# Kernel tuning notes

Measured on AMD Instinct MI355X. Metric: run time of the kernel, lower is better.

The kernel has to match this reference:

```python
import jax, jax.numpy as jnp
import numpy as np

D_MODEL = 512
N_HEADS = 8
BLOCK = 512
D_HEAD = D_MODEL // N_HEADS
SCALE = D_HEAD ** -0.5


def _linear_params(key, d_in, d_out):
    kw, kb = jax.random.split(key)
    bound = 1.0 / np.sqrt(d_in)
    w = jax.random.uniform(kw, (d_in, d_out), jnp.float32, -bound, bound)
    b = jax.random.uniform(kb, (d_out,), jnp.float32, -bound, bound)
    return w, b


def setup_inputs() -> dict:
    key = jax.random.key(0)
    keys = jax.random.split(key, 10)
    x = jax.random.normal(keys[0], (4, 8192, D_MODEL), jnp.float32)
    names = ["lq", "lk", "lv", "lo", "gq", "gk", "gv", "go"]
    inp = {"x": x}
    for i, n in enumerate(names):
        w, b = _linear_params(keys[1 + i], D_MODEL, D_MODEL)
        inp[n + "_w"] = w
        inp[n + "_b"] = b
    gw, gb = _linear_params(keys[9], 2 * D_MODEL, D_MODEL)
    inp["gate_w"] = gw
    inp["gate_b"] = gb
    return inp


def _attend(q, k, v):
    # q,k,v: (..., L, H, Dh) -> (..., L, H, Dh)
    scores = jnp.einsum("...qhd,...khd->...hqk", q, k) * SCALE
    probs = jax.nn.softmax(scores, axis=-1)
    return jnp.einsum("...hqk,...khd->...qhd", probs, v)


def reference(x, lq_w, lq_b, lk_w, lk_b, lv_w, lv_b, lo_w, lo_b,
              gq_w, gq_b, gk_w, gk_b, gv_w, gv_b, go_w, go_b,
              gate_w, gate_b):
    B, S, D = x.shape
    nb = S // BLOCK
    xb = x.reshape(B, nb, BLOCK, D)

    def heads(t, L_axes):
        return t.reshape(t.shape[:-1] + (N_HEADS, D_HEAD))

    # block-local attention (all blocks batched)
    Q = heads(xb @ lq_w + lq_b, None)  # (B, nb, bs, H, Dh)
    K = heads(xb @ lk_w + lk_b, None)
    V = heads(xb @ lv_w + lv_b, None)
    loc = _attend(Q, K, V).reshape(B, nb, BLOCK, D)
    local_out = (loc @ lo_w + lo_b).reshape(B, S, D)

    # pooled block summaries: AdaptiveAvgPool1d(1) == mean over block length
    pooled = xb.mean(axis=2)  # (B, nb, D)
    Qg = heads(pooled @ gq_w + gq_b, None)  # (B, nb, H, Dh)
    Kg = heads(pooled @ gk_w + gk_b, None)
    Vg = heads(pooled @ gv_w + gv_b, None)
    glob = _attend(Qg, Kg, Vg).reshape(B, nb, D)
    glob = glob @ go_w + go_b  # (B, nb, D)

    # broadcast each block summary to its tokens
    global_out = jnp.repeat(glob, BLOCK, axis=1)  # (B, S, D)

    gate_in = jnp.concatenate([local_out, global_out], axis=-1)
    gate = jax.nn.sigmoid(gate_in @ gate_w + gate_b)
    return gate * local_out + (1.0 - gate) * global_out
```

## Files before the change

kernel.cpp:

```cpp
#include <hip/hip_runtime.h>
#include <math.h>

typedef unsigned short u16;
typedef short s16;
typedef u16 u16x8 __attribute__((ext_vector_type(8)));
typedef u16 u16x4 __attribute__((ext_vector_type(4)));
typedef s16 s16x8 __attribute__((ext_vector_type(8)));
typedef float f32x4 __attribute__((ext_vector_type(4)));
typedef unsigned u32x4 __attribute__((ext_vector_type(4)));

__device__ __forceinline__ float b2f(u16 u) { return __uint_as_float(((unsigned)u) << 16); }
__device__ __forceinline__ u16 f2b(float f) {
  unsigned x = __float_as_uint(f);
  unsigned r = x + 0x7fffu + ((x >> 16) & 1u);
  return (u16)(r >> 16);
}
__device__ __forceinline__ unsigned cvtpk(float a, float b) {
  unsigned r;
  asm("v_cvt_pk_bf16_f32 %0, %1, %2" : "=v"(r) : "v"(a), "v"(b));
  return r;
}
union PkH { u32x4 w; s16x8 h; };
union Pk2 { unsigned w[2]; u16x4 h; };

#define SCALE 0.125f
#define SCLG2E 0.1803368801111137f
#define DM 512
#define NTOK 32768

typedef __attribute__((address_space(1))) unsigned int as1_u32;
typedef __attribute__((address_space(3))) unsigned int as3_u32;
__device__ __forceinline__ void gl2lds16(const u16* g, u16* s) {
  __builtin_amdgcn_global_load_lds((as1_u32*)g, (as3_u32*)s, 16, 0, 0);
}

__global__ __launch_bounds__(256)
void conv_psum(const float* __restrict__ X, u16* __restrict__ Xb,
               float* __restrict__ Psum)
{
  __shared__ float ps[4][512];
  const int tid = threadIdx.x;
  const int c8 = (tid & 63) * 8;
  const int rg = tid >> 6;
  const size_t tok0 = (size_t)blockIdx.x * 64;
  f32x4 s0 = {0.f, 0.f, 0.f, 0.f}, s1 = {0.f, 0.f, 0.f, 0.f};
  for (int it = 0; it < 16; ++it) {
    const size_t tok = tok0 + it * 4 + rg;
    const float* xp = X + tok * DM + c8;
    f32x4 a = *(const f32x4*)xp;
    f32x4 b = *(const f32x4*)(xp + 4);
    Pk2 p0, p1;
    p0.w[0] = cvtpk(a[0], a[1]); p0.w[1] = cvtpk(a[2], a[3]);
    p1.w[0] = cvtpk(b[0], b[1]); p1.w[1] = cvtpk(b[2], b[3]);
    *(u16x4*)(Xb + tok * DM + c8)     = p0.h;
    *(u16x4*)(Xb + tok * DM + c8 + 4) = p1.h;
    s0 += a; s1 += b;
  }
  *(f32x4*)&ps[rg][c8]     = s0;
  *(f32x4*)&ps[rg][c8 + 4] = s1;
  __syncthreads();
#pragma unroll
  for (int i = 0; i < 2; ++i) {
    const int col = tid + i * 256;
    Psum[(size_t)blockIdx.x * DM + col] =
        ps[0][col] + ps[1][col] + ps[2][col] + ps[3][col];
  }
}

__global__ __launch_bounds__(256)
void pool_prep(const float* __restrict__ Psum, u16* __restrict__ PB)
{
  const int g = blockIdx.x, tid = threadIdx.x;
#pragma unroll
  for (int i = 0; i < 2; ++i) {
    const int col = tid + i * 256;
    float v = 0.f;
#pragma unroll
    for (int s = 0; s < 8; ++s) v += Psum[(size_t)(g * 8 + s) * DM + col];
    PB[(size_t)g * DM + col] = f2b(v * (1.f / 512.f));
  }
}

__global__ __launch_bounds__(256)
void trans_w(const float* w0, const float* w1, const float* w2, const float* w3,
             const float* w4, const float* w5, const float* w6, const float* w7,
             const float* w8, const float* w9, u16* __restrict__ WT)
{
  __shared__ float t[32][33];
  const int z = blockIdx.z;
  const float* W = (z == 0) ? w0 : (z == 1) ? w1 : (z == 2) ? w2 : (z == 3) ? w3 :
                   (z == 4) ? w4 : (z == 5) ? w5 : (z == 6) ? w6 : (z == 7) ? w7 :
                   (z == 8) ? w8 : w9;
  u16* D = WT + (size_t)z * DM * DM;
  const int tx = threadIdx.x & 31, ty = threadIdx.x >> 5;
  const int n0 = blockIdx.x * 32, k0 = blockIdx.y * 32;
#pragma unroll
  for (int j = 0; j < 4; ++j)
    t[ty + j * 8][tx] = W[(size_t)(k0 + ty + j * 8) * DM + n0 + tx];
  __syncthreads();
#pragma unroll
  for (int j = 0; j < 4; ++j)
    D[(size_t)(n0 + ty + j * 8) * DM + k0 + tx] = f2b(t[tx][ty + j * 8]);
}

__global__ __launch_bounds__(256)
void conv_w(const float* __restrict__ W, u16* __restrict__ D)
{
  const size_t i = ((size_t)blockIdx.x * 256 + threadIdx.x) * 8;
  f32x4 a = *(const f32x4*)(W + i);
  f32x4 b = *(const f32x4*)(W + i + 4);
  Pk2 p0, p1;
  p0.w[0] = cvtpk(a[0], a[1]); p0.w[1] = cvtpk(a[2], a[3]);
  p1.w[0] = cvtpk(b[0], b[1]); p1.w[1] = cvtpk(b[2], b[3]);
  *(u16x4*)(D + i)     = p0.h;
  *(u16x4*)(D + i + 4) = p1.h;
}

__global__ __launch_bounds__(256)
void bc_kernel(const float* __restrict__ go_b, const float* __restrict__ gate_w,
               const float* __restrict__ gate_b, float* __restrict__ bc)
{
  __shared__ float red[8][32];
  const int tid = threadIdx.x;
  const int jj = tid & 31, part = tid >> 5;
  const int j = blockIdx.x * 32 + jj;
  float p = 0.f;
#pragma unroll
  for (int i = 0; i < 64; ++i) {
    const int k = part * 64 + i;
    p = fmaf(go_b[k], gate_w[(size_t)(512 + k) * DM + j], p);
  }
  red[part][jj] = p;
  __syncthreads();
  if (tid < 32) {
    float v = gate_b[blockIdx.x * 32 + tid];
#pragma unroll
    for (int s = 0; s < 8; ++s) v += red[s][tid];
    bc[blockIdx.x * 32 + tid] = v;
  }
}

__global__ __launch_bounds__(256)
void gemm_qkv(const u16* __restrict__ A,
              const u16* __restrict__ WTq, const u16* __restrict__ WTk,
              const u16* __restrict__ WTv,
              const float* __restrict__ bq, const float* __restrict__ bk,
              const float* __restrict__ bv,
              u16* __restrict__ Qb, u16* __restrict__ Kb, u16* __restrict__ VT)
{
  __shared__ u16 As[2][128 * 64];
  __shared__ u16 Bs[2][128 * 64];
  const int tid = threadIdx.x;
  const int w = tid >> 6, l = tid & 63;
  const int l15 = l & 15, gl = l >> 4;
  const int wm = w >> 1, wn = w & 1;

  const int H = blockIdx.y * 12 + blockIdx.x;
  const int xcd = H & 7, i = H >> 3;
  const int mt = xcd * 32 + i / 12;
  const int nt = i % 12;
  const int sel = nt >> 2;
  const int m0 = mt * 128;
  const int n0 = (nt & 3) * 128;

  const u16* Wt = (sel == 0) ? WTq : (sel == 1) ? WTk : WTv;
  const float* bias = (sel == 0) ? bq : (sel == 1) ? bk : bv;

  const int srow = l >> 3;
  const int scol = ((l & 7) ^ (srow & 7)) * 8;
  const u16* Ag = A  + (size_t)(m0 + w * 32 + srow) * DM + scol;
  const u16* Bg = Wt + (size_t)(n0 + w * 32 + srow) * DM + scol;

  auto stage = [&](int t, int b) {
    const int k0 = t * 64;
#pragma unroll
    for (int c = 0; c < 4; ++c) {
      gl2lds16(Ag + (size_t)(c * 8) * DM + k0, &As[b][(w * 32 + c * 8) * 64]);
      gl2lds16(Bg + (size_t)(c * 8) * DM + k0, &Bs[b][(w * 32 + c * 8) * 64]);
    }
  };

  f32x4 acc[4][4];
#pragma unroll
  for (int ii = 0; ii < 4; ++ii)
#pragma unroll
    for (int j = 0; j < 4; ++j) acc[ii][j] = {0.f, 0.f, 0.f, 0.f};

  const int xorv = l15 & 7;
  stage(0, 0);
#pragma unroll
  for (int t = 0; t < 8; ++t) {
    if (t < 7) {
      stage(t + 1, (t + 1) & 1);
      asm volatile("s_waitcnt vmcnt(8)" ::: "memory");
    } else {
      asm volatile("s_waitcnt vmcnt(0)" ::: "memory");
    }
    __builtin_amdgcn_s_barrier();
    __builtin_amdgcn_sched_barrier(0);
    const int b = t & 1;
#pragma unroll
    for (int kd = 0; kd < 2; ++kd) {
      const int go = ((gl + 4 * kd) ^ xorv) * 8;
      s16x8 af[4], bfr[4];
#pragma unroll
      for (int f = 0; f < 4; ++f) {
        af[f]  = *(const s16x8*)&As[b][(wm * 64 + f * 16 + l15) * 64 + go];
        bfr[f] = *(const s16x8*)&Bs[b][(wn * 64 + f * 16 + l15) * 64 + go];
      }
      if (sel == 2) {
#pragma unroll
        for (int fm = 0; fm < 4; ++fm)
#pragma unroll
          for (int fn = 0; fn < 4; ++fn)
            acc[fm][fn] = __builtin_amdgcn_mfma_f32_16x16x32_bf16(
                af[fm], bfr[fn], acc[fm][fn], 0, 0, 0);
      } else {
#pragma unroll
        for (int fm = 0; fm < 4; ++fm)
#pragma unroll
          for (int fn = 0; fn < 4; ++fn)
            acc[fm][fn] = __builtin_amdgcn_mfma_f32_16x16x32_bf16(
                bfr[fn], af[fm], acc[fm][fn], 0, 0, 0);
      }
    }
    __builtin_amdgcn_s_barrier();
  }

  if (sel == 2) {
#pragma unroll
    for (int fn = 0; fn < 4; ++fn) {
      const int n = n0 + wn * 64 + fn * 16 + l15;
      const float bn = bias[n];
      const int d = n & 63, ghn = n >> 6;
#pragma unroll
      for (int fm = 0; fm < 4; ++fm) {
        const int m = m0 + wm * 64 + fm * 16 + gl * 4;
        const int f = (m & 63) >> 4;
        const int pos = ((f >> 1) << 5) | (gl << 3) | ((f & 1) << 2);
        Pk2 p;
        p.w[0] = cvtpk(acc[fm][fn][0] + bn, acc[fm][fn][1] + bn);
        p.w[1] = cvtpk(acc[fm][fn][2] + bn, acc[fm][fn][3] + bn);
        *(u16x4*)(VT + ((size_t)(((m >> 9) * 8 + ghn) * 64 + d)) * 512
                     + ((m & 511) >> 6) * 64 + pos) = p.h;
      }
    }
  } else {
    u16* Cb = (sel == 0) ? Qb : Kb;
    const float sc = (sel == 0) ? SCLG2E : 1.0f;
#pragma unroll
    for (int fm = 0; fm < 4; ++fm) {
      const int m = m0 + wm * 64 + fm * 16 + l15;
#pragma unroll
      for (int fn = 0; fn < 4; ++fn) {
        const int nb = n0 + wn * 64 + fn * 16 + gl * 4;
        f32x4 b4 = *(const f32x4*)&bias[nb];
        f32x4 v = (acc[fm][fn] + b4) * sc;
        Pk2 p;
        p.w[0] = cvtpk(v[0], v[1]);
        p.w[1] = cvtpk(v[2], v[3]);
        *(u16x4*)(Cb + (size_t)m * DM + nb) = p.h;
      }
    }
  }
}

template<int EPI>
__global__ __launch_bounds__(256)
void gemm_mfma(const u16* __restrict__ A, const u16* __restrict__ Wt,
               const float* __restrict__ bias, u16* __restrict__ Cb,
               float* __restrict__ Cf, float outscale,
               const float* __restrict__ GG)
{
  __shared__ u16 As[2][128 * 64];
  __shared__ u16 Bs[2][128 * 64];
  const int tid = threadIdx.x;
  const int w = tid >> 6, l = tid & 63;
  const int l15 = l & 15, gl = l >> 4;
  const int wm = w >> 1, wn = w & 1;

  int mt, nt;
  if (gridDim.y == 256) {
    const int H = blockIdx.y * 4 + blockIdx.x;
    const int xcd = H & 7, i = H >> 3;
    mt = xcd * 32 + (i >> 2);
    nt = i & 3;
  } else {
    mt = blockIdx.y; nt = blockIdx.x;
  }
  const int m0 = mt * 128, n0 = nt * 128;

  const int srow = l >> 3;
  const int scol = ((l & 7) ^ (srow & 7)) * 8;
  const u16* Ag = A  + (size_t)(m0 + w * 32 + srow) * DM + scol;
  const u16* Bg = Wt + (size_t)(n0 + w * 32 + srow) * DM + scol;

  auto stage = [&](int t, int b) {
    const int k0 = t * 64;
#pragma unroll
    for (int c = 0; c < 4; ++c) {
      gl2lds16(Ag + (size_t)(c * 8) * DM + k0, &As[b][(w * 32 + c * 8) * 64]);
      gl2lds16(Bg + (size_t)(c * 8) * DM + k0, &Bs[b][(w * 32 + c * 8) * 64]);
    }
  };

  f32x4 acc[4][4];
#pragma unroll
  for (int i = 0; i < 4; ++i)
#pragma unroll
    for (int j = 0; j < 4; ++j) acc[i][j] = {0.f, 0.f, 0.f, 0.f};

  const int xorv = l15 & 7;
  stage(0, 0);
#pragma unroll
  for (int t = 0; t < 8; ++t) {
    if (t < 7) {
      stage(t + 1, (t + 1) & 1);
      asm volatile("s_waitcnt vmcnt(8)" ::: "memory");
    } else {
      asm volatile("s_waitcnt vmcnt(0)" ::: "memory");
    }
    __builtin_amdgcn_s_barrier();
    __builtin_amdgcn_sched_barrier(0);
    const int b = t & 1;
#pragma unroll
    for (int kd = 0; kd < 2; ++kd) {
      const int go = ((gl + 4 * kd) ^ xorv) * 8;
      s16x8 af[4], bfr[4];
#pragma unroll
      for (int f = 0; f < 4; ++f) {
        af[f]  = *(const s16x8*)&As[b][(wm * 64 + f * 16 + l15) * 64 + go];
        bfr[f] = *(const s16x8*)&Bs[b][(wn * 64 + f * 16 + l15) * 64 + go];
      }
#pragma unroll
      for (int fm = 0; fm < 4; ++fm)
#pragma unroll
        for (int fn = 0; fn < 4; ++fn)
          acc[fm][fn] = __builtin_amdgcn_mfma_f32_16x16x32_bf16(
              bfr[fn], af[fm], acc[fm][fn], 0, 0, 0);
    }
    __builtin_amdgcn_s_barrier();
  }

#pragma unroll
  for (int fm = 0; fm < 4; ++fm) {
    const int m = m0 + wm * 64 + fm * 16 + l15;
    const int brow = m >> 9;
#pragma unroll
    for (int fn = 0; fn < 4; ++fn) {
      const int nb = n0 + wn * 64 + fn * 16 + gl * 4;
      if (EPI == 0) {
        f32x4 b4 = *(const f32x4*)&bias[nb];
        f32x4 v = (acc[fm][fn] + b4) * outscale;
        Pk2 p;
        p.w[0] = cvtpk(v[0], v[1]);
        p.w[1] = cvtpk(v[2], v[3]);
        *(u16x4*)(Cb + (size_t)m * DM + nb) = p.h;
      } else if (EPI == 3) {
        Pk2 p;
        p.w[0] = cvtpk(acc[fm][fn][0], acc[fm][fn][1]);
        p.w[1] = cvtpk(acc[fm][fn][2], acc[fm][fn][3]);
        *(u16x4*)(Cb + (size_t)m * DM + nb) = p.h;
      } else {
        f32x4 z = acc[fm][fn] + *(const f32x4*)&GG[(size_t)brow * 1024 + 512 + nb];
        u16x4 lo4 = *(const u16x4*)(A + (size_t)m * DM + nb);
        f32x4 go4 = *(const f32x4*)&GG[(size_t)brow * 1024 + nb];
        f32x4 res;
#pragma unroll
        for (int r = 0; r < 4; ++r) {
          float g = 1.f / (1.f + __expf(-z[r]));
          res[r] = g * b2f(lo4[r]) + (1.f - g) * go4[r];
        }
        *(f32x4*)(Cf + (size_t)m * DM + nb) = res;
      }
    }
  }
}

__global__ __launch_bounds__(256)
void gemm64(const u16* __restrict__ A,
            const u16* B0, const u16* B1, const u16* B2,
            const float* b0, const float* b1, const float* b2,
            float* __restrict__ Out, int ldo)
{
  __shared__ u16 As[2][64 * 64];
  __shared__ u16 Bs[2][128 * 64];
  const int tid = threadIdx.x;
  const int w = tid >> 6, l = tid & 63;
  const int l15 = l & 15, gl = l >> 4;
  const int bx = blockIdx.x;
  const int grp = bx >> 2;
  const u16* Bt = ((grp == 0) ? B0 : (grp == 1) ? B1 : B2)
                  + (size_t)(bx & 3) * 128 * DM;
  const float* bias = (grp == 0) ? b0 : (grp == 1) ? b1 : b2;

  const int srow = l >> 3;
  const int scol = ((l & 7) ^ (srow & 7)) * 8;
  const u16* Ag = A  + (size_t)(w * 16 + srow) * DM + scol;
  const u16* Bg = Bt + (size_t)(w * 32 + srow) * DM + scol;

  auto stage = [&](int t, int b) {
    const int k0 = t * 64;
#pragma unroll
    for (int c = 0; c < 2; ++c)
      gl2lds16(Ag + (size_t)(c * 8) * DM + k0, &As[b][(w * 16 + c * 8) * 64]);
#pragma unroll
    for (int c = 0; c < 4; ++c)
      gl2lds16(Bg + (size_t)(c * 8) * DM + k0, &Bs[b][(w * 32 + c * 8) * 64]);
  };

  f32x4 acc[4][2];
#pragma unroll
  for (int i = 0; i < 4; ++i)
#pragma unroll
    for (int j = 0; j < 2; ++j) acc[i][j] = {0.f, 0.f, 0.f, 0.f};

  const int xorv = l15 & 7;
  stage(0, 0);
#pragma unroll
  for (int t = 0; t < 8; ++t) {
    if (t < 7) {
      stage(t + 1, (t + 1) & 1);
      asm volatile("s_waitcnt vmcnt(6)" ::: "memory");
    } else {
      asm volatile("s_waitcnt vmcnt(0)" ::: "memory");
    }
    __builtin_amdgcn_s_barrier();
    __builtin_amdgcn_sched_barrier(0);
    const int b = t & 1;
#pragma unroll
    for (int kd = 0; kd < 2; ++kd) {
      const int go = ((gl + 4 * kd) ^ xorv) * 8;
      s16x8 af[4], bfr[2];
#pragma unroll
      for (int f = 0; f < 4; ++f)
        af[f] = *(const s16x8*)&As[b][(f * 16 + l15) * 64 + go];
#pragma unroll
      for (int f = 0; f < 2; ++f)
        bfr[f] = *(const s16x8*)&Bs[b][(w * 32 + f * 16 + l15) * 64 + go];
#pragma unroll
      for (int fm = 0; fm < 4; ++fm)
#pragma unroll
        for (int fn = 0; fn < 2; ++fn)
          acc[fm][fn] = __builtin_amdgcn_mfma_f32_16x16x32_bf16(
              bfr[fn], af[fm], acc[fm][fn], 0, 0, 0);
    }
    __builtin_amdgcn_s_barrier();
  }

#pragma unroll
  for (int fm = 0; fm < 4; ++fm) {
    const int m = fm * 16 + l15;
#pragma unroll
    for (int fn = 0; fn < 2; ++fn) {
      const int nloc = w * 32 + fn * 16 + gl * 4;
      f32x4 b4 = *(const f32x4*)&bias[(bx & 3) * 128 + nloc];
      *(f32x4*)&Out[(size_t)m * ldo + bx * 128 + nloc] = acc[fm][fn] + b4;
    }
  }
}

__global__ __launch_bounds__(512, 4)
void attn_mfma(const u16* __restrict__ Q, const u16* __restrict__ K,
               const u16* __restrict__ VT, u16* __restrict__ CTX)
{
  __shared__ u16 Ks[64 * 64];
  __shared__ u16 VsT[64 * 64];
  const int tid = threadIdx.x;
  const int w = tid >> 6, l = tid & 63;
  const int l15 = l & 15, gl = l >> 4;
  const int g = blockIdx.x, h = blockIdx.y, qh = blockIdx.z;
  const int t0 = g * 512;
  const int fb = h * 64;
  const int q0 = t0 + qh * 256 + w * 32;
  const u16* VTb = VT + ((size_t)(g * 8 + h) * 64) * 512;

  s16x8 qf[2][2];
#pragma unroll
  for (int fq = 0; fq < 2; ++fq)
#pragma unroll
    for (int kd = 0; kd < 2; ++kd)
      qf[fq][kd] = *(const s16x8*)(Q + (size_t)(q0 + fq * 16 + l15) * DM
                                     + fb + gl * 8 + kd * 32);

  s16x8 vones;
#pragma unroll
  for (int j = 0; j < 8; ++j) vones[j] = (s16)0x3F80;

  f32x4 o[2][4];
#pragma unroll
  for (int i = 0; i < 2; ++i)
#pragma unroll
    for (int j = 0; j < 4; ++j) o[i][j] = {0.f, 0.f, 0.f, 0.f};
  f32x4 o_sum[2] = {{0.f,0.f,0.f,0.f}, {0.f,0.f,0.f,0.f}};

  const int srow = tid >> 3;
  const int swg = ((tid & 7) ^ ((tid >> 3) & 7)) * 8;
  const u16* Kg = K + (size_t)(t0 + srow) * DM + fb + swg;
  const u16* Vg = VTb + (size_t)srow * 512 + swg;
  s16x8 kreg = *(const s16x8*)Kg;
  s16x8 vreg = *(const s16x8*)Vg;
  const int sw = l15 & 7;

  for (int kc = 0; kc < 8; ++kc) {
    __syncthreads();
    *(s16x8*)&Ks[tid * 8]  = kreg;
    *(s16x8*)&VsT[tid * 8] = vreg;
    __syncthreads();
    if (kc < 7) {
      kreg = *(const s16x8*)(Kg + (size_t)(kc + 1) * 64 * DM);
      vreg = *(const s16x8*)(Vg + (kc + 1) * 64);
    }

    f32x4 s[4][2];
#pragma unroll
    for (int i = 0; i < 4; ++i)
#pragma unroll
      for (int j = 0; j < 2; ++j) s[i][j] = {0.f, 0.f, 0.f, 0.f};
#pragma unroll
    for (int kd = 0; kd < 2; ++kd) {
      s16x8 kf[4];
#pragma unroll
      for (int fm = 0; fm < 4; ++fm)
        kf[fm] = *(const s16x8*)&Ks[(fm * 16 + l15) * 64 + ((gl + 4 * kd) ^ sw) * 8];
#pragma unroll
      for (int fm = 0; fm < 4; ++fm)
#pragma unroll
        for (int fq = 0; fq < 2; ++fq)
          s[fm][fq] = __builtin_amdgcn_mfma_f32_16x16x32_bf16(
              kf[fm], qf[fq][kd], s[fm][fq], 0, 0, 0);
    }

#pragma unroll
    for (int fq = 0; fq < 2; ++fq)
#pragma unroll
      for (int fm = 0; fm < 4; ++fm)
#pragma unroll
        for (int r = 0; r < 4; ++r) s[fm][fq][r] = exp2f(s[fm][fq][r]);

    PkH pf[2][2];
#pragma unroll
    for (int ka = 0; ka < 2; ++ka)
#pragma unroll
      for (int fq = 0; fq < 2; ++fq) {
        pf[ka][fq].w[0] = cvtpk(s[2 * ka][fq][0], s[2 * ka][fq][1]);
        pf[ka][fq].w[1] = cvtpk(s[2 * ka][fq][2], s[2 * ka][fq][3]);
        pf[ka][fq].w[2] = cvtpk(s[2 * ka + 1][fq][0], s[2 * ka + 1][fq][1]);
        pf[ka][fq].w[3] = cvtpk(s[2 * ka + 1][fq][2], s[2 * ka + 1][fq][3]);
      }

#pragma unroll
    for (int ka = 0; ka < 2; ++ka) {
#pragma unroll
      for (int fd = 0; fd < 4; ++fd) {
        s16x8 vf = *(const s16x8*)&VsT[(fd * 16 + l15) * 64 + ((ka * 4 + gl) ^ sw) * 8];
#pragma unroll
        for (int qm = 0; qm < 2; ++qm)
          o[qm][fd] = __builtin_amdgcn_mfma_f32_16x16x32_bf16(
              pf[ka][qm].h, vf, o[qm][fd], 0, 0, 0);
      }
#pragma unroll
      for (int qm = 0; qm < 2; ++qm)
        o_sum[qm] = __builtin_amdgcn_mfma_f32_16x16x32_bf16(
            pf[ka][qm].h, vones, o_sum[qm], 0, 0, 0);
    }
  }

#pragma unroll
  for (int qm = 0; qm < 2; ++qm) {
    f32x4 inv4;
#pragma unroll
    for (int r = 0; r < 4; ++r) inv4[r] = 1.f / o_sum[qm][r];
#pragma unroll
    for (int fd = 0; fd < 4; ++fd) {
      const size_t base = (size_t)(q0 + qm * 16 + gl * 4) * DM + fb + fd * 16 + l15;
      CTX[base]          = f2b(o[qm][fd][0] * inv4[0]);
      CTX[base + DM]     = f2b(o[qm][fd][1] * inv4[1]);
      CTX[base + 2 * DM] = f2b(o[qm][fd][2] * inv4[2]);
      CTX[base + 3 * DM] = f2b(o[qm][fd][3] * inv4[3]);
    }
  }
}

__global__ __launch_bounds__(256)
void gattn(const float* __restrict__ QKVg, u16* __restrict__ GlB)
{
  __shared__ float q[16][64], k[16][64], v[16][64];
  __shared__ float sc[16][16];
  const int bh = blockIdx.x;
  const int b = bh >> 3, h = bh & 7;
  const int tid = threadIdx.x;
  for (int idx = tid; idx < 1024; idx += 256) {
    const int n = idx >> 6, d = idx & 63;
    const size_t off = (size_t)(b * 16 + n) * 1536 + h * 64 + d;
    q[n][d] = QKVg[off]; k[n][d] = QKVg[off + 512]; v[n][d] = QKVg[off + 1024];
  }
  __syncthreads();
  {
    const int qq = tid >> 4, kk = tid & 15;
    float s = 0.f;
#pragma unroll
    for (int d = 0; d < 64; ++d) s = fmaf(q[qq][d], k[kk][d], s);
    sc[qq][kk] = s * SCALE;
  }
  __syncthreads();
  if (tid < 16) {
    float mx = -INFINITY;
#pragma unroll
    for (int j = 0; j < 16; ++j) mx = fmaxf(mx, sc[tid][j]);
    float e[16]; float sum = 0.f;
#pragma unroll
    for (int j = 0; j < 16; ++j) { e[j] = __expf(sc[tid][j] - mx); sum += e[j]; }
    const float inv = 1.f / sum;
#pragma unroll
    for (int j = 0; j < 16; ++j) sc[tid][j] = e[j] * inv;
  }
  __syncthreads();
  for (int idx = tid; idx < 1024; idx += 256) {
    const int qq = idx >> 6, d = idx & 63;
    float o = 0.f;
#pragma unroll
    for (int j = 0; j < 16; ++j) o = fmaf(sc[qq][j], v[j][d], o);
    GlB[(size_t)(b * 16 + qq) * DM + h * 64 + d] = f2b(o);
  }
}

extern "C" void kernel_launch(void* const* d_in, const int* in_sizes, int n_in,
                              void* d_out, int out_size, void* d_ws, size_t ws_size,
                              hipStream_t stream)
{
  const float* x      = (const float*)d_in[0];
  const float* lq_w   = (const float*)d_in[1];
  const float* lq_b   = (const float*)d_in[2];
  const float* lk_w   = (const float*)d_in[3];
  const float* lk_b   = (const float*)d_in[4];
  const float* lv_w   = (const float*)d_in[5];
  const float* lv_b   = (const float*)d_in[6];
  const float* lo_w   = (const float*)d_in[7];
  const float* lo_b   = (const float*)d_in[8];
  const float* gq_w   = (const float*)d_in[9];
  const float* gq_b   = (const float*)d_in[10];
  const float* gk_w   = (const float*)d_in[11];
  const float* gk_b   = (const float*)d_in[12];
  const float* gv_w   = (const float*)d_in[13];
  const float* gv_b   = (const float*)d_in[14];
  const float* go_w   = (const float*)d_in[15];
  const float* go_b   = (const float*)d_in[16];
  const float* gate_w = (const float*)d_in[17];
  const float* gate_b = (const float*)d_in[18];
  float* out = (float*)d_out;

  const size_t NE = (size_t)NTOK * DM;
  const size_t DD = (size_t)DM * DM;
  char* ws = (char*)d_ws;
  u16* Qb  = (u16*)ws;
  u16* Kb  = Qb + NE;
  u16* VT  = Kb + NE;
  u16* WT  = VT + NE;
  u16* goD = WT + 10 * DD;
  u16* WcT = goD + DD;
  u16* PB  = WcT + DD;
  u16* GlB = PB + 64 * DM;
  float* scr  = (float*)(GlB + 64 * DM);
  float* Psum = scr;
  float* QKVg = Psum + 512 * DM;
  float* GG   = QKVg + (size_t)64 * 1536;
  float* bc   = GG + (size_t)64 * 1024;
  u16* xb = (u16*)d_out;
  u16* LOCAL = Kb;

  u16* WTq  = WT;
  u16* WTk  = WT + 1 * DD;
  u16* WTv  = WT + 2 * DD;
  u16* WTo  = WT + 3 * DD;
  u16* WTg  = WT + 4 * DD;
  u16* WTgq = WT + 5 * DD;
  u16* WTgk = WT + 6 * DD;
  u16* WTgv = WT + 7 * DD;
  u16* WTgo = WT + 8 * DD;
  u16* WTg2 = WT + 9 * DD;

  conv_psum<<<512, 256, 0, stream>>>(x, xb, Psum);
  trans_w<<<dim3(16, 16, 10), 256, 0, stream>>>(
      lq_w, lk_w, lv_w, lo_w, gate_w, gq_w, gk_w, gv_w, go_w,
      gate_w + DD, WT);
  conv_w<<<128, 256, 0, stream>>>(go_w, goD);
  bc_kernel<<<16, 256, 0, stream>>>(go_b, gate_w, gate_b, bc);
  pool_prep<<<64, 256, 0, stream>>>(Psum, PB);

  const dim3 gg(4, 256), bb(256);
  gemm_qkv<<<dim3(12, 256), bb, 0, stream>>>(xb, WTq, WTk, WTv,
                                             lq_b, lk_b, lv_b, Qb, Kb, VT);
  gemm_mfma<3><<<dim3(4, 4), bb, 0, stream>>>(WTg2, goD, nullptr, WcT, nullptr, 1.0f, nullptr);

  attn_mfma<<<dim3(64, 8, 2), 512, 0, stream>>>(Qb, Kb, VT, Qb );
  gemm_mfma<0><<<gg, bb, 0, stream>>>(Qb , WTo, lo_b, LOCAL, nullptr, 1.0f, nullptr);

  gemm64<<<12, 256, 0, stream>>>(PB, WTgq, WTgk, WTgv, gq_b, gk_b, gv_b, QKVg, 1536);
  gattn<<<32, 256, 0, stream>>>(QKVg, GlB);
  gemm64<<<8, 256, 0, stream>>>(GlB, WTgo, WcT, WcT, go_b, bc, bc, GG, 1024);

  gemm_mfma<1><<<gg, bb, 0, stream>>>(LOCAL, WTg, nullptr, nullptr, out, 1.0f, GG);
}
```

Before: 284.4 us.

## Fold output projection into gate weights and fuse output and gate GEMMs

```diff
diff --git a/kernel.cpp b/kernel.cpp
--- a/kernel.cpp
+++ b/kernel.cpp
@@ -117,8 +117,8 @@
 }
 
 __global__ __launch_bounds__(256)
-void bc_kernel(const float* __restrict__ go_b, const float* __restrict__ gate_w,
-               const float* __restrict__ gate_b, float* __restrict__ bc)
+void bc_kernel(const float* __restrict__ gb, const float* __restrict__ gate_w,
+               const float* __restrict__ addb, float* __restrict__ bc, int koff)
 {
   __shared__ float red[8][32];
   const int tid = threadIdx.x;
@@ -128,12 +128,12 @@
 #pragma unroll
   for (int i = 0; i < 64; ++i) {
     const int k = part * 64 + i;
-    p = fmaf(go_b[k], gate_w[(size_t)(512 + k) * DM + j], p);
+    p = fmaf(gb[k], gate_w[(size_t)(koff + k) * DM + j], p);
   }
   red[part][jj] = p;
   __syncthreads();
   if (tid < 32) {
-    float v = gate_b[blockIdx.x * 32 + tid];
+    float v = addb ? addb[blockIdx.x * 32 + tid] : 0.f;
 #pragma unroll
     for (int s = 0; s < 8; ++s) v += red[s][tid];
     bc[blockIdx.x * 32 + tid] = v;
@@ -141,12 +141,8 @@
 }
 
 __global__ __launch_bounds__(256)
-void gemm_qkv(const u16* __restrict__ A,
-              const u16* __restrict__ WTq, const u16* __restrict__ WTk,
-              const u16* __restrict__ WTv,
-              const float* __restrict__ bq, const float* __restrict__ bk,
-              const float* __restrict__ bv,
-              u16* __restrict__ Qb, u16* __restrict__ Kb, u16* __restrict__ VT)
+void gemm_comb(const u16* __restrict__ A, const u16* __restrict__ Wt,
+               u16* __restrict__ Cb)
 {
   __shared__ u16 As[2][128 * 64];
   __shared__ u16 Bs[2][128 * 64];
@@ -154,17 +150,7 @@
   const int w = tid >> 6, l = tid & 63;
   const int l15 = l & 15, gl = l >> 4;
   const int wm = w >> 1, wn = w & 1;
-
-  const int H = blockIdx.y * 12 + blockIdx.x;
-  const int xcd = H & 7, i = H >> 3;
-  const int mt = xcd * 32 + i / 12;
-  const int nt = i % 12;
-  const int sel = nt >> 2;
-  const int m0 = mt * 128;
-  const int n0 = (nt & 3) * 128;
-
-  const u16* Wt = (sel == 0) ? WTq : (sel == 1) ? WTk : WTv;
-  const float* bias = (sel == 0) ? bq : (sel == 1) ? bk : bv;
+  const int m0 = blockIdx.y * 128, n0 = blockIdx.x * 128;
 
   const int srow = l >> 3;
   const int scol = ((l & 7) ^ (srow & 7)) * 8;
@@ -182,9 +168,9 @@
 
   f32x4 acc[4][4];
 #pragma unroll
-  for (int ii = 0; ii < 4; ++ii)
-#pragma unroll
-    for (int j = 0; j < 4; ++j) acc[ii][j] = {0.f, 0.f, 0.f, 0.f};
+  for (int i = 0; i < 4; ++i)
+#pragma unroll
+    for (int j = 0; j < 4; ++j) acc[i][j] = {0.f, 0.f, 0.f, 0.f};
 
   const int xorv = l15 & 7;
   stage(0, 0);
@@ -208,69 +194,37 @@
         af[f]  = *(const s16x8*)&As[b][(wm * 64 + f * 16 + l15) * 64 + go];
         bfr[f] = *(const s16x8*)&Bs[b][(wn * 64 + f * 16 + l15) * 64 + go];
       }
-      if (sel == 2) {
-#pragma unroll
-        for (int fm = 0; fm < 4; ++fm)
-#pragma unroll
-          for (int fn = 0; fn < 4; ++fn)
-            acc[fm][fn] = __builtin_amdgcn_mfma_f32_16x16x32_bf16(
-                af[fm], bfr[fn], acc[fm][fn], 0, 0, 0);
-      } else {
-#pragma unroll
-        for (int fm = 0; fm < 4; ++fm)
-#pragma unroll
-          for (int fn = 0; fn < 4; ++fn)
-            acc[fm][fn] = __builtin_amdgcn_mfma_f32_16x16x32_bf16(
-                bfr[fn], af[fm], acc[fm][fn], 0, 0, 0);
-      }
+#pragma unroll
+      for (int fm = 0; fm < 4; ++fm)
+#pragma unroll
+        for (int fn = 0; fn < 4; ++fn)
+          acc[fm][fn] = __builtin_amdgcn_mfma_f32_16x16x32_bf16(
+              bfr[fn], af[fm], acc[fm][fn], 0, 0, 0);
     }
     __builtin_amdgcn_s_barrier();
   }
 
-  if (sel == 2) {
+#pragma unroll
+  for (int fm = 0; fm < 4; ++fm) {
+    const int m = m0 + wm * 64 + fm * 16 + l15;
 #pragma unroll
     for (int fn = 0; fn < 4; ++fn) {
-      const int n = n0 + wn * 64 + fn * 16 + l15;
-      const float bn = bias[n];
-      const int d = n & 63, ghn = n >> 6;
-#pragma unroll
-      for (int fm = 0; fm < 4; ++fm) {
-        const int m = m0 + wm * 64 + fm * 16 + gl * 4;
-        const int f = (m & 63) >> 4;
-        const int pos = ((f >> 1) << 5) | (gl << 3) | ((f & 1) << 2);
-        Pk2 p;
-        p.w[0] = cvtpk(acc[fm][fn][0] + bn, acc[fm][fn][1] + bn);
-        p.w[1] = cvtpk(acc[fm][fn][2] + bn, acc[fm][fn][3] + bn);
-        *(u16x4*)(VT + ((size_t)(((m >> 9) * 8 + ghn) * 64 + d)) * 512
-                     + ((m & 511) >> 6) * 64 + pos) = p.h;
-      }
-    }
-  } else {
-    u16* Cb = (sel == 0) ? Qb : Kb;
-    const float sc = (sel == 0) ? SCLG2E : 1.0f;
-#pragma unroll
-    for (int fm = 0; fm < 4; ++fm) {
-      const int m = m0 + wm * 64 + fm * 16 + l15;
-#pragma unroll
-      for (int fn = 0; fn < 4; ++fn) {
-        const int nb = n0 + wn * 64 + fn * 16 + gl * 4;
-        f32x4 b4 = *(const f32x4*)&bias[nb];
-        f32x4 v = (acc[fm][fn] + b4) * sc;
-        Pk2 p;
-        p.w[0] = cvtpk(v[0], v[1]);
-        p.w[1] = cvtpk(v[2], v[3]);
-        *(u16x4*)(Cb + (size_t)m * DM + nb) = p.h;
-      }
-    }
-  }
-}
-
-template<int EPI>
-__global__ __launch_bounds__(256)
-void gemm_mfma(const u16* __restrict__ A, const u16* __restrict__ Wt,
-               const float* __restrict__ bias, u16* __restrict__ Cb,
-               float* __restrict__ Cf, float outscale,
-               const float* __restrict__ GG)
+      const int nb = n0 + wn * 64 + fn * 16 + gl * 4;
+      Pk2 p;
+      p.w[0] = cvtpk(acc[fm][fn][0], acc[fm][fn][1]);
+      p.w[1] = cvtpk(acc[fm][fn][2], acc[fm][fn][3]);
+      *(u16x4*)(Cb + (size_t)m * DM + nb) = p.h;
+    }
+  }
+}
+
+__global__ __launch_bounds__(256)
+void gemm_qkv3(const u16* __restrict__ A,
+               const u16* __restrict__ WTq, const u16* __restrict__ WTk,
+               const u16* __restrict__ WTv,
+               const float* __restrict__ bq, const float* __restrict__ bk,
+               const float* __restrict__ bv,
+               u16* __restrict__ Qb, u16* __restrict__ Kb, u16* __restrict__ VT)
 {
   __shared__ u16 As[2][128 * 64];
   __shared__ u16 Bs[2][128 * 64];
@@ -279,67 +233,218 @@
   const int l15 = l & 15, gl = l >> 4;
   const int wm = w >> 1, wn = w & 1;
 
-  int mt, nt;
-  if (gridDim.y == 256) {
-    const int H = blockIdx.y * 4 + blockIdx.x;
-    const int xcd = H & 7, i = H >> 3;
-    mt = xcd * 32 + (i >> 2);
-    nt = i & 3;
-  } else {
-    mt = blockIdx.y; nt = blockIdx.x;
-  }
+  const int H = blockIdx.y * 4 + blockIdx.x;
+  const int xcd = H & 7, i = H >> 3;
+  const int mt = xcd * 32 + (i >> 2);
+  const int nt = i & 3;
   const int m0 = mt * 128, n0 = nt * 128;
 
   const int srow = l >> 3;
   const int scol = ((l & 7) ^ (srow & 7)) * 8;
-  const u16* Ag = A  + (size_t)(m0 + w * 32 + srow) * DM + scol;
-  const u16* Bg = Wt + (size_t)(n0 + w * 32 + srow) * DM + scol;
-
-  auto stage = [&](int t, int b) {
-    const int k0 = t * 64;
-#pragma unroll
-    for (int c = 0; c < 4; ++c) {
-      gl2lds16(Ag + (size_t)(c * 8) * DM + k0, &As[b][(w * 32 + c * 8) * 64]);
-      gl2lds16(Bg + (size_t)(c * 8) * DM + k0, &Bs[b][(w * 32 + c * 8) * 64]);
-    }
-  };
-
-  f32x4 acc[4][4];
-#pragma unroll
-  for (int i = 0; i < 4; ++i)
-#pragma unroll
-    for (int j = 0; j < 4; ++j) acc[i][j] = {0.f, 0.f, 0.f, 0.f};
-
+  const u16* Ag = A + (size_t)(m0 + w * 32 + srow) * DM + scol;
   const int xorv = l15 & 7;
-  stage(0, 0);
-#pragma unroll
-  for (int t = 0; t < 8; ++t) {
-    if (t < 7) {
-      stage(t + 1, (t + 1) & 1);
-      asm volatile("s_waitcnt vmcnt(8)" ::: "memory");
+
+  for (int pass = 0; pass < 3; ++pass) {
+    const u16* Wtp = (pass == 0) ? WTq : (pass == 1) ? WTk : WTv;
+    const float* bias = (pass == 0) ? bq : (pass == 1) ? bk : bv;
+    const u16* Bg = Wtp + (size_t)(n0 + w * 32 + srow) * DM + scol;
+
+    auto stage = [&](int t, int b) {
+      const int k0 = t * 64;
+#pragma unroll
+      for (int c = 0; c < 4; ++c) {
+        gl2lds16(Ag + (size_t)(c * 8) * DM + k0, &As[b][(w * 32 + c * 8) * 64]);
+        gl2lds16(Bg + (size_t)(c * 8) * DM + k0, &Bs[b][(w * 32 + c * 8) * 64]);
+      }
+    };
+
+    f32x4 acc[4][4];
+#pragma unroll
+    for (int ii = 0; ii < 4; ++ii)
+#pragma unroll
+      for (int j = 0; j < 4; ++j) acc[ii][j] = {0.f, 0.f, 0.f, 0.f};
+
+    stage(0, 0);
+    if (pass < 2) {
+#pragma unroll
+      for (int t = 0; t < 8; ++t) {
+        if (t < 7) {
+          stage(t + 1, (t + 1) & 1);
+          asm volatile("s_waitcnt vmcnt(8)" ::: "memory");
+        } else {
+          asm volatile("s_waitcnt vmcnt(0)" ::: "memory");
+        }
+        __builtin_amdgcn_s_barrier();
+        __builtin_amdgcn_sched_barrier(0);
+        const int b = t & 1;
+#pragma unroll
+        for (int kd = 0; kd < 2; ++kd) {
+          const int go = ((gl + 4 * kd) ^ xorv) * 8;
+          s16x8 af[4], bfr[4];
+#pragma unroll
+          for (int f = 0; f < 4; ++f) {
+            af[f]  = *(const s16x8*)&As[b][(wm * 64 + f * 16 + l15) * 64 + go];
+            bfr[f] = *(const s16x8*)&Bs[b][(wn * 64 + f * 16 + l15) * 64 + go];
+          }
+#pragma unroll
+          for (int fm = 0; fm < 4; ++fm)
+#pragma unroll
+            for (int fn = 0; fn < 4; ++fn)
+              acc[fm][fn] = __builtin_amdgcn_mfma_f32_16x16x32_bf16(
+                  bfr[fn], af[fm], acc[fm][fn], 0, 0, 0);
+        }
+        __builtin_amdgcn_s_barrier();
+      }
+      u16* Cb = (pass == 0) ? Qb : Kb;
+      const float sc = (pass == 0) ? SCLG2E : 1.0f;
+#pragma unroll
+      for (int fm = 0; fm < 4; ++fm) {
+        const int m = m0 + wm * 64 + fm * 16 + l15;
+#pragma unroll
+        for (int fn = 0; fn < 4; ++fn) {
+          const int nb = n0 + wn * 64 + fn * 16 + gl * 4;
+          f32x4 b4 = *(const f32x4*)&bias[nb];
+          f32x4 v = (acc[fm][fn] + b4) * sc;
+          Pk2 p;
+          p.w[0] = cvtpk(v[0], v[1]);
+          p.w[1] = cvtpk(v[2], v[3]);
+          *(u16x4*)(Cb + (size_t)m * DM + nb) = p.h;
+        }
+      }
     } else {
-      asm volatile("s_waitcnt vmcnt(0)" ::: "memory");
-    }
-    __builtin_amdgcn_s_barrier();
-    __builtin_amdgcn_sched_barrier(0);
-    const int b = t & 1;
-#pragma unroll
-    for (int kd = 0; kd < 2; ++kd) {
-      const int go = ((gl + 4 * kd) ^ xorv) * 8;
-      s16x8 af[4], bfr[4];
-#pragma unroll
-      for (int f = 0; f < 4; ++f) {
-        af[f]  = *(const s16x8*)&As[b][(wm * 64 + f * 16 + l15) * 64 + go];
-        bfr[f] = *(const s16x8*)&Bs[b][(wn * 64 + f * 16 + l15) * 64 + go];
-      }
-#pragma unroll
-      for (int fm = 0; fm < 4; ++fm)
-#pragma unroll
-        for (int fn = 0; fn < 4; ++fn)
-          acc[fm][fn] = __builtin_amdgcn_mfma_f32_16x16x32_bf16(
-              bfr[fn], af[fm], acc[fm][fn], 0, 0, 0);
-    }
-    __builtin_amdgcn_s_barrier();
+#pragma unroll
+      for (int t = 0; t < 8; ++t) {
+        if (t < 7) {
+          stage(t + 1, (t + 1) & 1);
+          asm volatile("s_waitcnt vmcnt(8)" ::: "memory");
+        } else {
+          asm volatile("s_waitcnt vmcnt(0)" ::: "memory");
+        }
+        __builtin_amdgcn_s_barrier();
+        __builtin_amdgcn_sched_barrier(0);
+        const int b = t & 1;
+#pragma unroll
+        for (int kd = 0; kd < 2; ++kd) {
+          const int go = ((gl + 4 * kd) ^ xorv) * 8;
+          s16x8 af[4], bfr[4];
+#pragma unroll
+          for (int f = 0; f < 4; ++f) {
+            af[f]  = *(const s16x8*)&As[b][(wm * 64 + f * 16 + l15) * 64 + go];
+            bfr[f] = *(const s16x8*)&Bs[b][(wn * 64 + f * 16 + l15) * 64 + go];
+          }
+#pragma unroll
+          for (int fm = 0; fm < 4; ++fm)
+#pragma unroll
+            for (int fn = 0; fn < 4; ++fn)
+              acc[fm][fn] = __builtin_amdgcn_mfma_f32_16x16x32_bf16(
+                  af[fm], bfr[fn], acc[fm][fn], 0, 0, 0);
+        }
+        __builtin_amdgcn_s_barrier();
+      }
+#pragma unroll
+      for (int fn = 0; fn < 4; ++fn) {
+        const int n = n0 + wn * 64 + fn * 16 + l15;
+        const float bn = bv[n];
+        const int d = n & 63, ghn = n >> 6;
+#pragma unroll
+        for (int fm = 0; fm < 4; ++fm) {
+          const int m = m0 + wm * 64 + fm * 16 + gl * 4;
+          const int f = (m & 63) >> 4;
+          const int pos = ((f >> 1) << 5) | (gl << 3) | ((f & 1) << 2);
+          Pk2 p;
+          p.w[0] = cvtpk(acc[fm][fn][0] + bn, acc[fm][fn][1] + bn);
+          p.w[1] = cvtpk(acc[fm][fn][2] + bn, acc[fm][fn][3] + bn);
+          *(u16x4*)(VT + ((size_t)(((m >> 9) * 8 + ghn) * 64 + d)) * 512
+                       + ((m & 511) >> 6) * 64 + pos) = p.h;
+        }
+      }
+    }
+  }
+}
+
+__global__ __launch_bounds__(256)
+void gemm_fuse(const u16* __restrict__ A, const u16* __restrict__ WtL,
+               const u16* __restrict__ WtZ, const float* __restrict__ lo_b,
+               const float* __restrict__ bc1, const float* __restrict__ GG,
+               float* __restrict__ out)
+{
+  __shared__ u16 As[2][128 * 64];
+  __shared__ u16 Bs[2][128 * 64];
+  const int tid = threadIdx.x;
+  const int w = tid >> 6, l = tid & 63;
+  const int l15 = l & 15, gl = l >> 4;
+  const int wm = w >> 1, wn = w & 1;
+
+  const int H = blockIdx.y * 4 + blockIdx.x;
+  const int xcd = H & 7, i = H >> 3;
+  const int mt = xcd * 32 + (i >> 2);
+  const int nt = i & 3;
+  const int m0 = mt * 128, n0 = nt * 128;
+
+  const int srow = l >> 3;
+  const int scol = ((l & 7) ^ (srow & 7)) * 8;
+  const u16* Ag = A + (size_t)(m0 + w * 32 + srow) * DM + scol;
+  const int xorv = l15 & 7;
+
+  f32x4 accL[4][4], accZ[4][4];
+#pragma unroll
+  for (int ii = 0; ii < 4; ++ii)
+#pragma unroll
+    for (int j = 0; j < 4; ++j) {
+      accL[ii][j] = {0.f, 0.f, 0.f, 0.f};
+      accZ[ii][j] = {0.f, 0.f, 0.f, 0.f};
+    }
+
+  for (int pass = 0; pass < 2; ++pass) {
+    const u16* Wtp = (pass == 0) ? WtL : WtZ;
+    const u16* Bg = Wtp + (size_t)(n0 + w * 32 + srow) * DM + scol;
+    auto stage = [&](int t, int b) {
+      const int k0 = t * 64;
+#pragma unroll
+      for (int c = 0; c < 4; ++c) {
+        gl2lds16(Ag + (size_t)(c * 8) * DM + k0, &As[b][(w * 32 + c * 8) * 64]);
+        gl2lds16(Bg + (size_t)(c * 8) * DM + k0, &Bs[b][(w * 32 + c * 8) * 64]);
+      }
+    };
+    stage(0, 0);
+#pragma unroll
+    for (int t = 0; t < 8; ++t) {
+      if (t < 7) {
+        stage(t + 1, (t + 1) & 1);
+        asm volatile("s_waitcnt vmcnt(8)" ::: "memory");
+      } else {
+        asm volatile("s_waitcnt vmcnt(0)" ::: "memory");
+      }
+      __builtin_amdgcn_s_barrier();
+      __builtin_amdgcn_sched_barrier(0);
+      const int b = t & 1;
+#pragma unroll
+      for (int kd = 0; kd < 2; ++kd) {
+        const int go = ((gl + 4 * kd) ^ xorv) * 8;
+        s16x8 af[4], bfr[4];
+#pragma unroll
+        for (int f = 0; f < 4; ++f) {
+          af[f]  = *(const s16x8*)&As[b][(wm * 64 + f * 16 + l15) * 64 + go];
+          bfr[f] = *(const s16x8*)&Bs[b][(wn * 64 + f * 16 + l15) * 64 + go];
+        }
+        if (pass == 0) {
+#pragma unroll
+          for (int fm = 0; fm < 4; ++fm)
+#pragma unroll
+            for (int fn = 0; fn < 4; ++fn)
+              accL[fm][fn] = __builtin_amdgcn_mfma_f32_16x16x32_bf16(
+                  bfr[fn], af[fm], accL[fm][fn], 0, 0, 0);
+        } else {
+#pragma unroll
+          for (int fm = 0; fm < 4; ++fm)
+#pragma unroll
+            for (int fn = 0; fn < 4; ++fn)
+              accZ[fm][fn] = __builtin_amdgcn_mfma_f32_16x16x32_bf16(
+                  bfr[fn], af[fm], accZ[fm][fn], 0, 0, 0);
+        }
+      }
+      __builtin_amdgcn_s_barrier();
+    }
   }
 
 #pragma unroll
@@ -349,30 +454,17 @@
 #pragma unroll
     for (int fn = 0; fn < 4; ++fn) {
       const int nb = n0 + wn * 64 + fn * 16 + gl * 4;
-      if (EPI == 0) {
-        f32x4 b4 = *(const f32x4*)&bias[nb];
-        f32x4 v = (acc[fm][fn] + b4) * outscale;
-        Pk2 p;
-        p.w[0] = cvtpk(v[0], v[1]);
-        p.w[1] = cvtpk(v[2], v[3]);
-        *(u16x4*)(Cb + (size_t)m * DM + nb) = p.h;
-      } else if (EPI == 3) {
-        Pk2 p;
-        p.w[0] = cvtpk(acc[fm][fn][0], acc[fm][fn][1]);
-        p.w[1] = cvtpk(acc[fm][fn][2], acc[fm][fn][3]);
-        *(u16x4*)(Cb + (size_t)m * DM + nb) = p.h;
-      } else {
-        f32x4 z = acc[fm][fn] + *(const f32x4*)&GG[(size_t)brow * 1024 + 512 + nb];
-        u16x4 lo4 = *(const u16x4*)(A + (size_t)m * DM + nb);
-        f32x4 go4 = *(const f32x4*)&GG[(size_t)brow * 1024 + nb];
-        f32x4 res;
-#pragma unroll
-        for (int r = 0; r < 4; ++r) {
-          float g = 1.f / (1.f + __expf(-z[r]));
-          res[r] = g * b2f(lo4[r]) + (1.f - g) * go4[r];
-        }
-        *(f32x4*)(Cf + (size_t)m * DM + nb) = res;
-      }
+      f32x4 lo = accL[fm][fn] + *(const f32x4*)&lo_b[nb];
+      f32x4 z  = accZ[fm][fn] + *(const f32x4*)&bc1[nb]
+                 + *(const f32x4*)&GG[(size_t)brow * 1024 + 512 + nb];
+      f32x4 go4 = *(const f32x4*)&GG[(size_t)brow * 1024 + nb];
+      f32x4 res;
+#pragma unroll
+      for (int r = 0; r < 4; ++r) {
+        float g = 1.f / (1.f + __expf(-z[r]));
+        res[r] = g * lo[r] + (1.f - g) * go4[r];
+      }
+      *(f32x4*)(out + (size_t)m * DM + nb) = res;
     }
   }
 }
@@ -483,16 +575,12 @@
       qf[fq][kd] = *(const s16x8*)(Q + (size_t)(q0 + fq * 16 + l15) * DM
                                      + fb + gl * 8 + kd * 32);
 
-  s16x8 vones;
-#pragma unroll
-  for (int j = 0; j < 8; ++j) vones[j] = (s16)0x3F80;
-
   f32x4 o[2][4];
 #pragma unroll
   for (int i = 0; i < 2; ++i)
 #pragma unroll
     for (int j = 0; j < 4; ++j) o[i][j] = {0.f, 0.f, 0.f, 0.f};
-  f32x4 o_sum[2] = {{0.f,0.f,0.f,0.f}, {0.f,0.f,0.f,0.f}};
+  f32x4 psv[2] = {{0.f,0.f,0.f,0.f}, {0.f,0.f,0.f,0.f}};
 
   const int srow = tid >> 3;
   const int swg = ((tid & 7) ^ ((tid >> 3) & 7)) * 8;
@@ -534,9 +622,11 @@
 #pragma unroll
     for (int fq = 0; fq < 2; ++fq)
 #pragma unroll
-      for (int fm = 0; fm < 4; ++fm)
+      for (int fm = 0; fm < 4; ++fm) {
 #pragma unroll
         for (int r = 0; r < 4; ++r) s[fm][fq][r] = exp2f(s[fm][fq][r]);
+        psv[fq] += s[fm][fq];
+      }
 
     PkH pf[2][2];
 #pragma unroll
@@ -550,34 +640,34 @@
       }
 
 #pragma unroll
-    for (int ka = 0; ka < 2; ++ka) {
+    for (int ka = 0; ka < 2; ++ka)
 #pragma unroll
       for (int fd = 0; fd < 4; ++fd) {
         s16x8 vf = *(const s16x8*)&VsT[(fd * 16 + l15) * 64 + ((ka * 4 + gl) ^ sw) * 8];
 #pragma unroll
         for (int qm = 0; qm < 2; ++qm)
           o[qm][fd] = __builtin_amdgcn_mfma_f32_16x16x32_bf16(
-              pf[ka][qm].h, vf, o[qm][fd], 0, 0, 0);
-      }
-#pragma unroll
-      for (int qm = 0; qm < 2; ++qm)
-        o_sum[qm] = __builtin_amdgcn_mfma_f32_16x16x32_bf16(
-            pf[ka][qm].h, vones, o_sum[qm], 0, 0, 0);
-    }
-  }
-
+              vf, pf[ka][qm].h, o[qm][fd], 0, 0, 0);
+      }
+  }
+
+  float l_[2];
+#pragma unroll
+  for (int fq = 0; fq < 2; ++fq) {
+    float t = (psv[fq][0] + psv[fq][1]) + (psv[fq][2] + psv[fq][3]);
+    t += __shfl_xor(t, 16);
+    t += __shfl_xor(t, 32);
+    l_[fq] = t;
+  }
 #pragma unroll
   for (int qm = 0; qm < 2; ++qm) {
-    f32x4 inv4;
-#pragma unroll
-    for (int r = 0; r < 4; ++r) inv4[r] = 1.f / o_sum[qm][r];
+    const float inv = 1.f / l_[qm];
 #pragma unroll
     for (int fd = 0; fd < 4; ++fd) {
-      const size_t base = (size_t)(q0 + qm * 16 + gl * 4) * DM + fb + fd * 16 + l15;
-      CTX[base]          = f2b(o[qm][fd][0] * inv4[0]);
-      CTX[base + DM]     = f2b(o[qm][fd][1] * inv4[1]);
-      CTX[base + 2 * DM] = f2b(o[qm][fd][2] * inv4[2]);
-      CTX[base + 3 * DM] = f2b(o[qm][fd][3] * inv4[3]);
+      Pk2 p;
+      p.w[0] = cvtpk(o[qm][fd][0] * inv, o[qm][fd][1] * inv);
+      p.w[1] = cvtpk(o[qm][fd][2] * inv, o[qm][fd][3] * inv);
+      *(u16x4*)(CTX + (size_t)(q0 + qm * 16 + l15) * DM + fb + fd * 16 + gl * 4) = p.h;
     }
   }
 }
@@ -653,21 +743,23 @@
   const size_t NE = (size_t)NTOK * DM;
   const size_t DD = (size_t)DM * DM;
   char* ws = (char*)d_ws;
-  u16* Qb  = (u16*)ws;
-  u16* Kb  = Qb + NE;
-  u16* VT  = Kb + NE;
-  u16* WT  = VT + NE;
-  u16* goD = WT + 10 * DD;
-  u16* WcT = goD + DD;
-  u16* PB  = WcT + DD;
-  u16* GlB = PB + 64 * DM;
+  u16* Qb   = (u16*)ws;
+  u16* Kb   = Qb + NE;
+  u16* VT   = Kb + NE;
+  u16* WT   = VT + NE;
+  u16* goD  = WT + 10 * DD;
+  u16* loD  = goD + DD;
+  u16* WcT  = loD + DD;
+  u16* Wc1T = WcT + DD;
+  u16* PB   = Wc1T + DD;
+  u16* GlB  = PB + 64 * DM;
   float* scr  = (float*)(GlB + 64 * DM);
   float* Psum = scr;
   float* QKVg = Psum + 512 * DM;
   float* GG   = QKVg + (size_t)64 * 1536;
   float* bc   = GG + (size_t)64 * 1024;
+  float* bc1  = bc + DM;
   u16* xb = (u16*)d_out;
-  u16* LOCAL = Kb;
 
   u16* WTq  = WT;
   u16* WTk  = WT + 1 * DD;
@@ -685,20 +777,22 @@
       lq_w, lk_w, lv_w, lo_w, gate_w, gq_w, gk_w, gv_w, go_w,
       gate_w + DD, WT);
   conv_w<<<128, 256, 0, stream>>>(go_w, goD);
-  bc_kernel<<<16, 256, 0, stream>>>(go_b, gate_w, gate_b, bc);
+  conv_w<<<128, 256, 0, stream>>>(lo_w, loD);
+  bc_kernel<<<16, 256, 0, stream>>>(go_b, gate_w, gate_b, bc, 512);
+  bc_kernel<<<16, 256, 0, stream>>>(lo_b, gate_w, nullptr, bc1, 0);
   pool_prep<<<64, 256, 0, stream>>>(Psum, PB);
 
-  const dim3 gg(4, 256), bb(256);
-  gemm_qkv<<<dim3(12, 256), bb, 0, stream>>>(xb, WTq, WTk, WTv,
+  const dim3 bb(256);
+  gemm_qkv3<<<dim3(4, 256), bb, 0, stream>>>(xb, WTq, WTk, WTv,
                                              lq_b, lk_b, lv_b, Qb, Kb, VT);
-  gemm_mfma<3><<<dim3(4, 4), bb, 0, stream>>>(WTg2, goD, nullptr, WcT, nullptr, 1.0f, nullptr);
+  gemm_comb<<<dim3(4, 4), bb, 0, stream>>>(WTg2, goD, WcT);
+  gemm_comb<<<dim3(4, 4), bb, 0, stream>>>(WTg, loD, Wc1T);
 
   attn_mfma<<<dim3(64, 8, 2), 512, 0, stream>>>(Qb, Kb, VT, Qb );
-  gemm_mfma<0><<<gg, bb, 0, stream>>>(Qb , WTo, lo_b, LOCAL, nullptr, 1.0f, nullptr);
 
   gemm64<<<12, 256, 0, stream>>>(PB, WTgq, WTgk, WTgv, gq_b, gk_b, gv_b, QKVg, 1536);
   gattn<<<32, 256, 0, stream>>>(QKVg, GlB);
   gemm64<<<8, 256, 0, stream>>>(GlB, WTgo, WcT, WcT, go_b, bc, bc, GG, 1024);
 
-  gemm_mfma<1><<<gg, bb, 0, stream>>>(LOCAL, WTg, nullptr, nullptr, out, 1.0f, GG);
-}
+  gemm_fuse<<<dim3(4, 256), bb, 0, stream>>>(Qb , WTo, Wc1T, lo_b, bc1, GG, out);
+}
```

Result: slower. 314.3 us (+10.5%).
